# Kernel tuning notes

Hardware: AMD Instinct MI355X
Metric: run time of the kernel (lower is better)

The kernel has to match this reference:

```python
import jax
import jax.numpy as jnp
from jax import lax
import numpy as np

B, T, V, C = 64, 64, 64, 65  # batch, src_len, tgt_len, n_target_classes (vocab table: 1 + 2*32)


def setup_inputs() -> dict:
    key = jax.random.key(0)
    k1, k2, k3, k4 = jax.random.split(key, 4)
    # action_scores are log-probabilities over edit-operation classes per (t, v) cell
    action_scores = jax.nn.log_softmax(
        jax.random.normal(k1, (B, T, V, C), dtype=jnp.float32), axis=-1)
    all_deletion_ids = jax.random.randint(k2, (B, T), 0, C)
    all_insertion_ids = jax.random.randint(k3, (B, V), 0, C)
    all_subs_ids = jax.random.randint(k4, (B, T, V), 0, C)
    return {
        "action_scores": action_scores,
        "all_deletion_ids": all_deletion_ids,
        "all_insertion_ids": all_insertion_ids,
        "all_subs_ids": all_subs_ids,
    }


def _gather_scores(action_scores, all_deletion_ids, all_insertion_ids, all_subs_ids):
    b, t, v, c = action_scores.shape
    # deletion id depends only on t, insertion id only on v, substitution on (t, v)
    del_idx = jnp.broadcast_to(all_deletion_ids[:, :, None, None], (b, t, v, 1))
    ins_idx = jnp.broadcast_to(all_insertion_ids[:, None, :, None], (b, t, v, 1))
    sub_idx = all_subs_ids[:, :, :, None]
    dsc = jnp.take_along_axis(action_scores, del_idx, axis=3)[..., 0]  # [B,T,V]
    isc = jnp.take_along_axis(action_scores, ins_idx, axis=3)[..., 0]  # [B,T,V]
    ssc = jnp.take_along_axis(action_scores, sub_idx, axis=3)[..., 0]  # [B,T,V]
    return dsc, isc, ssc


def _forward_alpha(dsc, isc, ssc):
    """Edit-distance forward DP in log space.

    alpha[t, v] = logsumexp(ins[t,v] + alpha[t,v-1],
                            del[t,v] + alpha[t-1,v],
                            sub[t,v] + alpha[t-1,v-1]),  alpha[0,0] = 0.
    """
    b = dsc.shape[0]
    # Row t = 0: only insertions -> cumulative sum of insertion scores.
    alpha0 = jnp.cumsum(isc[:, 0, :].at[:, 0].set(0.0), axis=1)  # [B, V]

    def outer(prev_row, xs):
        d, i, s = xs  # each [B, V]
        # Terms coming from the previous row (fully parallel over v).
        base0 = d[:, 0] + prev_row[:, 0]                                   # [B]
        base_rest = jnp.logaddexp(d[:, 1:] + prev_row[:, 1:],
                                  s[:, 1:] + prev_row[:, :-1])             # [B, V-1]

        # Sequential within-row insertion recurrence: a[v] = lse(base[v], ins[v] + a[v-1])
        def inner(a_prev, bv):
            base_v, ins_v = bv
            a = jnp.logaddexp(base_v, ins_v + a_prev)
            return a, a

        _, rest = lax.scan(inner, base0,
                           (base_rest.transpose(1, 0), i[:, 1:].transpose(1, 0)))
        row = jnp.concatenate([base0[:, None], rest.transpose(1, 0)], axis=1)  # [B, V]
        return row, row

    xs = (dsc[:, 1:].transpose(1, 0, 2),
          isc[:, 1:].transpose(1, 0, 2),
          ssc[:, 1:].transpose(1, 0, 2))
    _, rows = lax.scan(outer, alpha0, xs)  # [T-1, B, V]
    alpha = jnp.concatenate([alpha0[None], rows], axis=0).transpose(1, 0, 2)  # [B, T, V]
    return alpha


def reference(action_scores, all_deletion_ids, all_insertion_ids, all_subs_ids):
    dsc, isc, ssc = _gather_scores(action_scores, all_deletion_ids,
                                   all_insertion_ids, all_subs_ids)
    return _forward_alpha(dsc, isc, ssc)
```

## Files before the change

kernel.cpp:

```cpp
#include <hip/hip_runtime.h>
#include <cstddef>

static constexpr int B = 64, T = 64, V = 64, C = 65;
static constexpr float NEG   = -1.0e30f;
static constexpr float LOG2E = 1.44269504088896340736f;
static constexpr float LN2   = 0.69314718055994530942f;

__device__ __forceinline__ float fexp2(float x) {
    float r; asm("v_exp_f32 %0, %1" : "=v"(r) : "v"(x)); return r;
}
__device__ __forceinline__ float flog2(float x) {
    float r; asm("v_log_f32 %0, %1" : "=v"(r) : "v"(x)); return r;
}

__device__ __forceinline__ float shr1(float x, int negi) {
    return __int_as_float(__builtin_amdgcn_update_dpp(
        negi, __float_as_int(x), 0x138 , 0xf, 0xf, false));
}

__global__ void __launch_bounds__(192) gather_kernel(
    const float* __restrict__ as,
    const int* __restrict__ del_ids,
    const int* __restrict__ ins_ids,
    const int* __restrict__ sub_ids,
    float* __restrict__ g)
{
    const int bt = blockIdx.x, b = bt >> 6, t = bt & 63;
    const int tid = threadIdx.x, v = tid & 63, kind = tid >> 6;
    int id;
    if (kind == 0)      id = del_ids[bt];
    else if (kind == 1) id = ins_ids[b * V + v];
    else                id = sub_ids[bt * V + v];
    const float val = as[(size_t)(bt * V + v) * C + id] * LOG2E;
    g[((b * 3 + kind) * T + t) * V + v] = val;
}

__global__ void __launch_bounds__(256) dp_kernel(
    const float* __restrict__ g, float* __restrict__ out)
{
    __shared__ float sc[3 * T * V];
    __shared__ float sAd[127 * V + V];

    const int b = blockIdx.x, tid = threadIdx.x;

    {
        const float4* __restrict__ src = (const float4*)(g + (size_t)b * 3 * T * V);
        float4* dst = (float4*)sc;
        #pragma unroll
        for (int j = 0; j < 12; ++j) dst[tid + j * 256] = src[tid + j * 256];
    }
    if (tid == 0) sAd[0] = 0.0f;
    __syncthreads();

    if (tid < 64) {
        const int v = tid;
        const int negi = __float_as_int(NEG);
        float a1 = (v == 0) ? 0.0f : NEG;
        float a2 = NEG;

        constexpr int PD = 7;
        float pD[PD], pI[PD], pS[PD];
        #pragma unroll
        for (int k = 0; k < PD; ++k) {
            const int tc = min(max(1 + k - v, 0), T - 1);
            const int off = tc * V + v;
            pD[k] = sc[off]; pI[k] = sc[T*V + off]; pS[k] = sc[2*T*V + off];
        }

        for (int gq = 0; gq < 17; ++gq) {
            #pragma unroll
            for (int k = 0; k < PD; ++k) {
                const int d = gq * PD + 1 + k;
                const float lf1 = shr1(a1, negi);
                const float lf2 = shr1(a2, negi);
                const float xd = pD[k] + a1;
                const float xs = pS[k] + lf2;
                const float xi = pI[k] + lf1;
                {
                    const int tc = min(max(d + PD - v, 0), T - 1);
                    const int off = tc * V + v;
                    pD[k] = sc[off]; pI[k] = sc[T*V + off]; pS[k] = sc[2*T*V + off];
                }
                const float m = fmaxf(fmaxf(xd, xs), xi);
                const float s = fexp2(xd - m) + fexp2(xs - m) + fexp2(xi - m);
                const float a = m + flog2(s);
                sAd[d * V + v] = a;
                a2 = a1; a1 = a;
            }
        }
        #pragma unroll
        for (int k = 0; k < PD; ++k) {
            const int d = 120 + k;
            const float lf1 = shr1(a1, negi);
            const float lf2 = shr1(a2, negi);
            const float xd = pD[k] + a1;
            const float xs = pS[k] + lf2;
            const float xi = pI[k] + lf1;
            const float m = fmaxf(fmaxf(xd, xs), xi);
            const float s = fexp2(xd - m) + fexp2(xs - m) + fexp2(xi - m);
            const float a = m + flog2(s);
            sAd[d * V + v] = a;
            a2 = a1; a1 = a;
        }
    }
    __syncthreads();

    {
        #pragma unroll
        for (int j = 0; j < 4; ++j) {
            const int idx = tid + j * 256;
            const int t = idx >> 4, v4 = (idx & 15) * 4;
            float4 r;
            r.x = sAd[(t + v4 + 0) * V + v4 + 0] * LN2;
            r.y = sAd[(t + v4 + 1) * V + v4 + 1] * LN2;
            r.z = sAd[(t + v4 + 2) * V + v4 + 2] * LN2;
            r.w = sAd[(t + v4 + 3) * V + v4 + 3] * LN2;
            ((float4*)out)[(size_t)b * 1024 + idx] = r;
        }
    }
}

extern "C" void kernel_launch(void* const* d_in, const int* in_sizes, int n_in,
                              void* d_out, int out_size, void* d_ws, size_t ws_size,
                              hipStream_t stream) {
    const float* as      = (const float*)d_in[0];
    const int*   del_ids = (const int*)d_in[1];
    const int*   ins_ids = (const int*)d_in[2];
    const int*   sub_ids = (const int*)d_in[3];
    float*       out     = (float*)d_out;
    float*       g       = (float*)d_ws;

    gather_kernel<<<B * T, 192, 0, stream>>>(as, del_ids, ins_ids, sub_ids, g);
    dp_kernel<<<B, 256, 0, stream>>>(g, out);
}
```

Measured before the change: 24.64 us.

## Fuse gather and DP kernels using per-batch atomic flag synchronization

Merges the gather and DP launches into one kernel. Each batch has four blocks that gather scores into workspace and then increment a per-batch counter; block 0 of each batch spin-waits on the counter, stages the gathered data into LDS and runs the DP. This is meant to remove the second kernel launch and the gap between kernels. In exchange it adds a memset launch and a spin-wait, and it depends on all four blocks of a batch being co-resident, which holds here with 256 blocks. The old two-kernel path stays as a fallback when the workspace is too small.

```diff
diff --git a/kernel.cpp b/kernel.cpp
--- a/kernel.cpp
+++ b/kernel.cpp
@@ -2,6 +2,7 @@
 #include <cstddef>
 
 static constexpr int B = 64, T = 64, V = 64, C = 65;
+static constexpr int NB = 4;
 static constexpr float NEG   = -1.0e30f;
 static constexpr float LOG2E = 1.44269504088896340736f;
 static constexpr float LN2   = 0.69314718055994530942f;
@@ -12,17 +13,139 @@
 __device__ __forceinline__ float flog2(float x) {
     float r; asm("v_log_f32 %0, %1" : "=v"(r) : "v"(x)); return r;
 }
-
 __device__ __forceinline__ float shr1(float x, int negi) {
     return __int_as_float(__builtin_amdgcn_update_dpp(
         negi, __float_as_int(x), 0x138 , 0xf, 0xf, false));
 }
 
-__global__ void __launch_bounds__(192) gather_kernel(
+
+__device__ __forceinline__ void dp_stage(const float* __restrict__ gsrc,
+                                         float* __restrict__ sc, int tid) {
+    const float4* __restrict__ src = (const float4*)gsrc;
+    float4* dst = (float4*)sc;
+    #pragma unroll
+    for (int j = 0; j < 12; ++j) dst[tid + j * 256] = src[tid + j * 256];
+}
+
+__device__ __forceinline__ void dp_chain(const float* __restrict__ sc,
+                                         float* __restrict__ sAd, int v) {
+    const int negi = __float_as_int(NEG);
+    float a1 = (v == 0) ? 0.0f : NEG;
+    float a2 = NEG;
+    constexpr int PD = 7;
+    float pD[PD], pI[PD], pS[PD];
+    #pragma unroll
+    for (int k = 0; k < PD; ++k) {
+        const int tc = min(max(1 + k - v, 0), T - 1);
+        const int off = tc * V + v;
+        pD[k] = sc[off]; pI[k] = sc[T*V + off]; pS[k] = sc[2*T*V + off];
+    }
+    for (int gq = 0; gq < 17; ++gq) {
+        #pragma unroll
+        for (int k = 0; k < PD; ++k) {
+            const int d = gq * PD + 1 + k;
+            const float lf1 = shr1(a1, negi);
+            const float lf2 = shr1(a2, negi);
+            const float xd = pD[k] + a1;
+            const float xs = pS[k] + lf2;
+            const float xi = pI[k] + lf1;
+            {
+                const int tc = min(max(d + PD - v, 0), T - 1);
+                const int off = tc * V + v;
+                pD[k] = sc[off]; pI[k] = sc[T*V + off]; pS[k] = sc[2*T*V + off];
+            }
+            const float m = fmaxf(fmaxf(xd, xs), xi);
+            const float s = fexp2(xd - m) + fexp2(xs - m) + fexp2(xi - m);
+            const float a = m + flog2(s);
+            sAd[d * V + v] = a;
+            a2 = a1; a1 = a;
+        }
+    }
+    #pragma unroll
+    for (int k = 0; k < PD; ++k) {
+        const int d = 120 + k;
+        const float lf1 = shr1(a1, negi);
+        const float lf2 = shr1(a2, negi);
+        const float xd = pD[k] + a1;
+        const float xs = pS[k] + lf2;
+        const float xi = pI[k] + lf1;
+        const float m = fmaxf(fmaxf(xd, xs), xi);
+        const float s = fexp2(xd - m) + fexp2(xs - m) + fexp2(xi - m);
+        const float a = m + flog2(s);
+        sAd[d * V + v] = a;
+        a2 = a1; a1 = a;
+    }
+}
+
+__device__ __forceinline__ void dp_writeout(const float* __restrict__ sAd,
+                                            float* __restrict__ out, int b, int tid) {
+    #pragma unroll
+    for (int j = 0; j < 4; ++j) {
+        const int idx = tid + j * 256;
+        const int t = idx >> 4, v4 = (idx & 15) * 4;
+        float4 r;
+        r.x = sAd[(t + v4 + 0) * V + v4 + 0] * LN2;
+        r.y = sAd[(t + v4 + 1) * V + v4 + 1] * LN2;
+        r.z = sAd[(t + v4 + 2) * V + v4 + 2] * LN2;
+        r.w = sAd[(t + v4 + 3) * V + v4 + 3] * LN2;
+        ((float4*)out)[(size_t)b * 1024 + idx] = r;
+    }
+}
+
+__global__ void __launch_bounds__(256) fused_kernel(
     const float* __restrict__ as,
     const int* __restrict__ del_ids,
     const int* __restrict__ ins_ids,
     const int* __restrict__ sub_ids,
+    float* __restrict__ g,
+    int* __restrict__ flags,
+    float* __restrict__ out)
+{
+    __shared__ __align__(16) float sc[3 * T * V];
+    __shared__ __align__(16) float sAd[128 * V];
+    const int b = blockIdx.x >> 2, j = blockIdx.x & (NB - 1);
+    const int tid = threadIdx.x;
+
+    {
+        const int base = j * 3072;
+        #pragma unroll
+        for (int k = 0; k < 12; ++k) {
+            const int p = base + k * 256 + tid;
+            const int kind = p >> 12, rem = p & 4095;
+            const int t = rem >> 6, v = rem & 63;
+            int id;
+            if (kind == 0)      id = del_ids[b * T + t];
+            else if (kind == 1) id = ins_ids[b * V + v];
+            else                id = sub_ids[(b * T + t) * V + v];
+            g[b * 12288 + p] = as[(size_t)((b * T + t) * V + v) * C + id] * LOG2E;
+        }
+    }
+    __syncthreads();
+    if (tid == 0) {
+        __threadfence();
+        atomicAdd(flags + b, 1);
+    }
+    if (j != 0) return;
+
+    if (tid == 0) {
+        while (__hip_atomic_load(flags + b, __ATOMIC_RELAXED,
+                                 __HIP_MEMORY_SCOPE_AGENT) < NB)
+            __builtin_amdgcn_s_sleep(4);
+        __threadfence();
+    }
+    __syncthreads();
+    dp_stage(g + b * 12288, sc, tid);
+    if (tid == 0) sAd[0] = 0.0f;
+    __syncthreads();
+    if (tid < 64) dp_chain(sc, sAd, tid);
+    __syncthreads();
+    dp_writeout(sAd, out, b, tid);
+}
+
+
+__global__ void __launch_bounds__(192) gather_kernel(
+    const float* __restrict__ as, const int* __restrict__ del_ids,
+    const int* __restrict__ ins_ids, const int* __restrict__ sub_ids,
     float* __restrict__ g)
 {
     const int bt = blockIdx.x, b = bt >> 6, t = bt & 63;
@@ -31,93 +154,22 @@
     if (kind == 0)      id = del_ids[bt];
     else if (kind == 1) id = ins_ids[b * V + v];
     else                id = sub_ids[bt * V + v];
-    const float val = as[(size_t)(bt * V + v) * C + id] * LOG2E;
-    g[((b * 3 + kind) * T + t) * V + v] = val;
+    g[((b * 3 + kind) * T + t) * V + v] =
+        as[(size_t)(bt * V + v) * C + id] * LOG2E;
 }
 
 __global__ void __launch_bounds__(256) dp_kernel(
     const float* __restrict__ g, float* __restrict__ out)
 {
-    __shared__ float sc[3 * T * V];
-    __shared__ float sAd[127 * V + V];
-
+    __shared__ __align__(16) float sc[3 * T * V];
+    __shared__ __align__(16) float sAd[128 * V];
     const int b = blockIdx.x, tid = threadIdx.x;
-
-    {
-        const float4* __restrict__ src = (const float4*)(g + (size_t)b * 3 * T * V);
-        float4* dst = (float4*)sc;
-        #pragma unroll
-        for (int j = 0; j < 12; ++j) dst[tid + j * 256] = src[tid + j * 256];
-    }
+    dp_stage(g + (size_t)b * 12288, sc, tid);
     if (tid == 0) sAd[0] = 0.0f;
     __syncthreads();
-
-    if (tid < 64) {
-        const int v = tid;
-        const int negi = __float_as_int(NEG);
-        float a1 = (v == 0) ? 0.0f : NEG;
-        float a2 = NEG;
-
-        constexpr int PD = 7;
-        float pD[PD], pI[PD], pS[PD];
-        #pragma unroll
-        for (int k = 0; k < PD; ++k) {
-            const int tc = min(max(1 + k - v, 0), T - 1);
-            const int off = tc * V + v;
-            pD[k] = sc[off]; pI[k] = sc[T*V + off]; pS[k] = sc[2*T*V + off];
-        }
-
-        for (int gq = 0; gq < 17; ++gq) {
-            #pragma unroll
-            for (int k = 0; k < PD; ++k) {
-                const int d = gq * PD + 1 + k;
-                const float lf1 = shr1(a1, negi);
-                const float lf2 = shr1(a2, negi);
-                const float xd = pD[k] + a1;
-                const float xs = pS[k] + lf2;
-                const float xi = pI[k] + lf1;
-                {
-                    const int tc = min(max(d + PD - v, 0), T - 1);
-                    const int off = tc * V + v;
-                    pD[k] = sc[off]; pI[k] = sc[T*V + off]; pS[k] = sc[2*T*V + off];
-                }
-                const float m = fmaxf(fmaxf(xd, xs), xi);
-                const float s = fexp2(xd - m) + fexp2(xs - m) + fexp2(xi - m);
-                const float a = m + flog2(s);
-                sAd[d * V + v] = a;
-                a2 = a1; a1 = a;
-            }
-        }
-        #pragma unroll
-        for (int k = 0; k < PD; ++k) {
-            const int d = 120 + k;
-            const float lf1 = shr1(a1, negi);
-            const float lf2 = shr1(a2, negi);
-            const float xd = pD[k] + a1;
-            const float xs = pS[k] + lf2;
-            const float xi = pI[k] + lf1;
-            const float m = fmaxf(fmaxf(xd, xs), xi);
-            const float s = fexp2(xd - m) + fexp2(xs - m) + fexp2(xi - m);
-            const float a = m + flog2(s);
-            sAd[d * V + v] = a;
-            a2 = a1; a1 = a;
-        }
-    }
+    if (tid < 64) dp_chain(sc, sAd, tid);
     __syncthreads();
-
-    {
-        #pragma unroll
-        for (int j = 0; j < 4; ++j) {
-            const int idx = tid + j * 256;
-            const int t = idx >> 4, v4 = (idx & 15) * 4;
-            float4 r;
-            r.x = sAd[(t + v4 + 0) * V + v4 + 0] * LN2;
-            r.y = sAd[(t + v4 + 1) * V + v4 + 1] * LN2;
-            r.z = sAd[(t + v4 + 2) * V + v4 + 2] * LN2;
-            r.w = sAd[(t + v4 + 3) * V + v4 + 3] * LN2;
-            ((float4*)out)[(size_t)b * 1024 + idx] = r;
-        }
-    }
+    dp_writeout(sAd, out, b, tid);
 }
 
 extern "C" void kernel_launch(void* const* d_in, const int* in_sizes, int n_in,
@@ -129,7 +181,15 @@
     const int*   sub_ids = (const int*)d_in[3];
     float*       out     = (float*)d_out;
     float*       g       = (float*)d_ws;
+    const size_t gbytes  = (size_t)B * 3 * T * V * sizeof(float);
 
-    gather_kernel<<<B * T, 192, 0, stream>>>(as, del_ids, ins_ids, sub_ids, g);
-    dp_kernel<<<B, 256, 0, stream>>>(g, out);
+    if (ws_size >= gbytes + 64 * sizeof(int)) {
+        int* flags = (int*)((char*)d_ws + gbytes);
+        hipMemsetAsync(flags, 0, 64 * sizeof(int), stream);
+        fused_kernel<<<B * NB, 256, 0, stream>>>(as, del_ids, ins_ids, sub_ids,
+                                                 g, flags, out);
+    } else {
+        gather_kernel<<<B * T, 192, 0, stream>>>(as, del_ids, ins_ids, sub_ids, g);
+        dp_kernel<<<B, 256, 0, stream>>>(g, out);
+    }
 }
```

After: 49.56 us. 101% more time.
